# Kernel tuning notes

Hardware: AMD Instinct MI355X
Metric: run time of the kernel (lower is better)

## Reference

```python
import jax, jax.numpy as jnp
import numpy as np

B, T, E, H = 64, 2048, 256, 512


def setup_inputs() -> dict:
    key = jax.random.key(0)
    ks = jax.random.split(key, 8)
    s_in = 1.0 / np.sqrt(E)
    s_h = 1.0 / np.sqrt(H)
    return {
        "x": jax.random.normal(ks[0], (B, T, E), jnp.float32),
        "lengths": jax.random.randint(ks[1], (B,), 1, T + 1, jnp.int32),
        "W_ih": jax.random.normal(ks[2], (H, E), jnp.float32) * s_in,
        "W_hh": jax.random.normal(ks[3], (H, H), jnp.float32) * s_h,
        "b_ih": jax.random.normal(ks[4], (H,), jnp.float32) * s_h,
        "b_hh": jax.random.normal(ks[5], (H,), jnp.float32) * s_h,
        "w_fc": jax.random.normal(ks[6], (1, H), jnp.float32) * s_h,
        "b_fc": jax.random.normal(ks[7], (1,), jnp.float32) * s_h,
    }


def reference(x, lengths, W_ih, W_hh, b_ih, b_hh, w_fc, b_fc):
    # Batched vanilla RNN (tanh), h0 = 0 (init_hidden in the original is dead code).
    b, t, _ = x.shape
    h = W_hh.shape[0]
    # Precompute input projections: [B,T,H] -> scan over time.
    xin = jnp.einsum('bte,he->bth', x, W_ih) + b_ih + b_hh

    def step(h_prev, x_t):
        h_new = jnp.tanh(x_t + h_prev @ W_hh.T)
        return h_new, h_new

    h0 = jnp.zeros((b, h), x.dtype)
    _, hs = jax.lax.scan(step, h0, jnp.swapaxes(xin, 0, 1))  # [T,B,H]
    hs = jnp.swapaxes(hs, 0, 1)  # [B,T,H]

    # fcn: Linear(H,1)+ReLU; count positives over valid (t < length) steps.
    logits = jnp.einsum('bth,oh->bto', hs, w_fc) + b_fc  # [B,T,1]
    valid = (jnp.arange(t)[None, :, None] < lengths[:, None, None])
    outs = jnp.sum((logits > 0) & valid, axis=1).astype(jnp.int32)  # [B,1]

    # h_n: hidden state at the last valid step of each sample.
    idx = jnp.clip(lengths - 1, 0, t - 1)
    h_n = hs[jnp.arange(b), idx]  # [B,H]
    h_n = jnp.where((lengths > 0)[:, None], h_n, jnp.zeros_like(h_n))
    return outs, h_n
```

## Files before the change

kernel.cpp:

```cpp
#include <hip/hip_runtime.h>
#include <stdint.h>

#define BB 64
#define TT 2048
#define EE 256
#define HH 512
#define SLICE 128
#define HXN (BB * 2 * HH)

typedef unsigned long long u64;
typedef float f32x4 __attribute__((ext_vector_type(4)));

__device__ __forceinline__ u64 pack_vt(float v, unsigned tag) {
    return ((u64)tag << 32) | (u64)__float_as_uint(v);
}

__global__ __attribute__((amdgpu_flat_work_group_size(256, 256),
                          amdgpu_waves_per_eu(1, 1)))
void rnn_scan(const float* __restrict__ x,
              const int* __restrict__ lengths,
              const float* __restrict__ W_ih,
              const float* __restrict__ W_hh,
              const float* __restrict__ b_ih,
              const float* __restrict__ b_hh,
              const float* __restrict__ w_fc,
              const float* __restrict__ b_fc,
              float* __restrict__ out,
              u64* __restrict__ hx)
{
    const int b   = blockIdx.x & 63;
    const int s   = blockIdx.x >> 6;
    const int tid = threadIdx.x;
    const int rg  = tid >> 3;
    const int kg  = tid & 7;
    const int row0 = s * SLICE + rg * 4;

    __shared__ float lds_h[2][HH];
    __shared__ float lds_x[2][EE];
    __shared__ float lds_wf[HH];

    f32x4 whh[4][16];
#pragma unroll
    for (int j = 0; j < 4; ++j)
#pragma unroll
        for (int i = 0; i < 16; ++i) {
            const int q = (i + kg) & 15;
            whh[j][i] = *(const f32x4*)&W_hh[(size_t)(row0 + j) * HH + kg * 64 + q * 4];
            asm volatile("" : "+a"(whh[j][i]));
        }
    f32x4 wih[4][8];
#pragma unroll
    for (int j = 0; j < 4; ++j)
#pragma unroll
        for (int i = 0; i < 8; ++i) {
            const int q = (i + kg) & 7;
            wih[j][i] = *(const f32x4*)&W_ih[(size_t)(row0 + j) * EE + kg * 32 + q * 4];
            asm volatile("" : "+v"(wih[j][i]));
        }
    const int pr0 = row0 + (kg & 1) * 2;
    const float bs0 = b_ih[pr0] + b_hh[pr0];
    const float bs1 = b_ih[pr0 + 1] + b_hh[pr0 + 1];
    float bfc = 0.f;
    if (s == 0 && tid < 64) bfc = b_fc[0];
    lds_wf[tid]       = w_fc[tid];
    lds_wf[tid + 256] = w_fc[tid + 256];

    const int len = lengths[b];
    const float* xrow = x + (size_t)b * TT * EE;
    u64* hxb = hx + (size_t)b * 2 * HH;

    lds_h[0][tid]       = 0.f;
    lds_h[0][tid + 256] = 0.f;
    if (tid < 64) *(f32x4*)&lds_x[0][tid * 4] = *(const f32x4*)&xrow[tid * 4];
    __syncthreads();

    int count = 0;

#pragma unroll 1
    for (int t = 0; t < len; ++t) {
        const int p = t & 1;
        const int si = tid - 192;
        f32x4 xn = {0.f, 0.f, 0.f, 0.f};
        if (si >= 0 && t + 1 < TT)
            xn = *(const f32x4*)&xrow[(size_t)(t + 1) * EE + si * 4];

        const float* hb = &lds_h[p][kg * 64];
        const float* xb = &lds_x[p][kg * 32];
        f32x4 a0 = {0.f,0.f,0.f,0.f}, a1 = a0, a2 = a0, a3 = a0;
#define FMA4(acc, w, v) \
        acc[0] = fmaf((w)[0], (v)[0], acc[0]); acc[1] = fmaf((w)[1], (v)[1], acc[1]); \
        acc[2] = fmaf((w)[2], (v)[2], acc[2]); acc[3] = fmaf((w)[3], (v)[3], acc[3]);
#pragma unroll
        for (int i = 0; i < 16; ++i) {
            f32x4 hv = *(const f32x4*)(hb + ((i + kg) & 15) * 4);
            FMA4(a0, whh[0][i], hv) FMA4(a1, whh[1][i], hv)
            FMA4(a2, whh[2][i], hv) FMA4(a3, whh[3][i], hv)
        }
#pragma unroll
        for (int i = 0; i < 8; ++i) {
            f32x4 xv = *(const f32x4*)(xb + ((i + kg) & 7) * 4);
            FMA4(a0, wih[0][i], xv) FMA4(a1, wih[1][i], xv)
            FMA4(a2, wih[2][i], xv) FMA4(a3, wih[3][i], xv)
        }
        float r0 = (a0[0] + a0[1]) + (a0[2] + a0[3]);
        float r1 = (a1[0] + a1[1]) + (a1[2] + a1[3]);
        float r2 = (a2[0] + a2[1]) + (a2[2] + a2[3]);
        float r3 = (a3[0] + a3[1]) + (a3[2] + a3[3]);
#pragma unroll
        for (int m = 1; m < 8; m <<= 1) {
            r0 += __shfl_xor(r0, m); r1 += __shfl_xor(r1, m);
            r2 += __shfl_xor(r2, m); r3 += __shfl_xor(r3, m);
        }

        const unsigned tag = (unsigned)(t + 1);
        u64* slot = hxb + (size_t)p * HH;

        if (kg < 2) {
            const float h0 = tanhf((kg ? r2 : r0) + bs0);
            const float h1 = tanhf((kg ? r3 : r1) + bs1);
            const int gi = pr0;
            *(float2*)&lds_h[p ^ 1][gi] = make_float2(h0, h1);
            __hip_atomic_store(&slot[gi], pack_vt(h0, tag),
                               __ATOMIC_RELAXED, __HIP_MEMORY_SCOPE_AGENT);
            __hip_atomic_store(&slot[gi + 1], pack_vt(h1, tag),
                               __ATOMIC_RELAXED, __HIP_MEMORY_SCOPE_AGENT);
        }

        if (tid < 192) {
            const int sp = (s + 1 + (tid >> 6)) & 3;
            const int gi = sp * SLICE + (tid & 63) * 2;
            u64 v0, v1;
            int g = 0;
            do { v0 = __hip_atomic_load(&slot[gi], __ATOMIC_RELAXED,
                                        __HIP_MEMORY_SCOPE_AGENT);
            } while ((unsigned)(v0 >> 32) != tag && ++g < (1 << 22));
            g = 0;
            do { v1 = __hip_atomic_load(&slot[gi + 1], __ATOMIC_RELAXED,
                                        __HIP_MEMORY_SCOPE_AGENT);
            } while ((unsigned)(v1 >> 32) != tag && ++g < (1 << 22));
            *(float2*)&lds_h[p ^ 1][gi] =
                make_float2(__uint_as_float((unsigned)v0),
                            __uint_as_float((unsigned)v1));
        } else if (t + 1 < TT) {
            *(f32x4*)&lds_x[p ^ 1][si * 4] = xn;
        }
        __syncthreads();

        if (s == 0) {
            if (tid < 64) {
                const f32x4* h4  = (const f32x4*)lds_h[p ^ 1];
                const f32x4* wf4 = (const f32x4*)lds_wf;
                f32x4 v0 = h4[tid * 2], v1 = h4[tid * 2 + 1];
                f32x4 w0 = wf4[tid * 2], w1 = wf4[tid * 2 + 1];
                float pd = v0[0]*w0[0] + v0[1]*w0[1] + v0[2]*w0[2] + v0[3]*w0[3]
                         + v1[0]*w1[0] + v1[1]*w1[1] + v1[2]*w1[2] + v1[3]*w1[3];
#pragma unroll
                for (int m = 1; m < 64; m <<= 1) pd += __shfl_xor(pd, m);
                if (tid == 0 && (pd + bfc) > 0.f) count++;
            }
            if (t == len - 1) {
                *(float2*)&out[64 + b * HH + tid * 2] =
                    *(const float2*)&lds_h[p ^ 1][tid * 2];
            }
        }
    }

    if (s == 0 && tid == 0) out[b] = (float)count;
}

extern "C" void kernel_launch(void* const* d_in, const int* in_sizes, int n_in,
                              void* d_out, int out_size, void* d_ws, size_t ws_size,
                              hipStream_t stream) {
    const float* x       = (const float*)d_in[0];
    const int*   lengths = (const int*)  d_in[1];
    const float* W_ih    = (const float*)d_in[2];
    const float* W_hh    = (const float*)d_in[3];
    const float* b_ih    = (const float*)d_in[4];
    const float* b_hh    = (const float*)d_in[5];
    const float* w_fc    = (const float*)d_in[6];
    const float* b_fc    = (const float*)d_in[7];
    float* out = (float*)d_out;
    u64*   hx  = (u64*)d_ws;

    hipLaunchKernelGGL(rnn_scan, dim3(BB * 4), dim3(256), 0, stream,
                       x, lengths, W_ih, W_hh, b_ih, b_hh, w_fc, b_fc, out, hx);
}
```

Baseline: 6.667 ms.

## Co-locate each batch's slices on one XCD and poll via vectorized L2 loads

At startup each workgroup reads its XCD id and claims a (batch, slice) slot through global atomic counters, so the four slices of a batch tend to land on the same XCD and share its L2. When they do, the per-step hidden-state exchange uses 16-byte stores and sc0 loads that poll both tagged values at once. If polling misses too often, it falls back to the original per-element atomic polling. This adds a bootstrap spin barrier across all 256 workgroups and a memset launch, and assumes every workgroup is resident at the same time.

```diff
diff --git a/kernel.cpp b/kernel.cpp
--- a/kernel.cpp
+++ b/kernel.cpp
@@ -9,10 +9,28 @@
 #define HXN (BB * 2 * HH)
 
 typedef unsigned long long u64;
+typedef u64 u64x2 __attribute__((ext_vector_type(2)));
 typedef float f32x4 __attribute__((ext_vector_type(4)));
 
 __device__ __forceinline__ u64 pack_vt(float v, unsigned tag) {
     return ((u64)tag << 32) | (u64)__float_as_uint(v);
+}
+__device__ __forceinline__ void st_l2_x4(u64* p, u64x2 v) {
+    asm volatile("global_store_dwordx4 %0, %1, off" :: "v"((u64)p), "v"(v) : "memory");
+}
+__device__ __forceinline__ u64x2 ld_l2_x4(const u64* p) {
+    u64x2 v;
+    asm volatile("global_load_dwordx4 %0, %1, off sc0\n\ts_waitcnt vmcnt(0)"
+                 : "=v"(v) : "v"((u64)p) : "memory");
+    return v;
+}
+__device__ __forceinline__ void barrier_lds(void) {
+    asm volatile("s_waitcnt lgkmcnt(0)\n\ts_barrier" ::: "memory");
+}
+
+#define AGENT __HIP_MEMORY_SCOPE_AGENT
+__device__ __forceinline__ unsigned a_add(unsigned* p, unsigned v, int mo) {
+    return __hip_atomic_fetch_add(p, v, mo, AGENT);
 }
 
 __global__ __attribute__((amdgpu_flat_work_group_size(256, 256),
@@ -28,16 +46,56 @@
               float* __restrict__ out,
               u64* __restrict__ hx)
 {
-    const int b   = blockIdx.x & 63;
-    const int s   = blockIdx.x >> 6;
     const int tid = threadIdx.x;
     const int rg  = tid >> 3;
     const int kg  = tid & 7;
-    const int row0 = s * SLICE + rg * 4;
 
     __shared__ float lds_h[2][HH];
     __shared__ float lds_x[2][EE];
     __shared__ float lds_wf[HH];
+    __shared__ int sh_batch, sh_slice, sh_fast, sh_miss;
+
+    if (tid == 0) {
+        unsigned xcd;
+        asm volatile("s_getreg_b32 %0, hwreg(HW_REG_XCC_ID)" : "=s"(xcd));
+        xcd &= 7u;
+        unsigned* boot = (unsigned*)(hx + HXN);
+        unsigned* cnt   = boot;
+        unsigned* total = boot + 8;
+        unsigned* ovfc  = boot + 9;
+        unsigned* bp1   = boot + 16;
+        unsigned* clm   = boot + 80;
+        unsigned my = a_add(&cnt[xcd], 1u, __ATOMIC_RELAXED);
+        int batch = -1, slice = 0, p1 = 0;
+        if (my < 32u) {
+            unsigned slot = xcd * 32u + my;
+            batch = (int)(slot >> 2); slice = (int)(slot & 3u); p1 = 1;
+            __hip_atomic_store(&clm[slot], 1u, __ATOMIC_RELAXED, AGENT);
+            a_add(&bp1[batch], 1u, __ATOMIC_RELAXED);
+        }
+        a_add(total, 1u, __ATOMIC_RELEASE);
+        int g = 0;
+        while (__hip_atomic_load(total, __ATOMIC_ACQUIRE, AGENT) < 256u &&
+               ++g < (1 << 26)) {}
+        if (!p1) {
+            unsigned k = a_add(ovfc, 1u, __ATOMIC_RELAXED);
+            unsigned seen = 0, slot = 0;
+            for (unsigned i2 = 0; i2 < 256u; ++i2) {
+                if (!__hip_atomic_load(&clm[i2], __ATOMIC_RELAXED, AGENT)) {
+                    if (seen == k) { slot = i2; break; }
+                    ++seen;
+                }
+            }
+            batch = (int)(slot >> 2); slice = (int)(slot & 3u);
+        }
+        const int fast =
+            (__hip_atomic_load(&bp1[batch], __ATOMIC_RELAXED, AGENT) == 4u);
+        sh_batch = batch; sh_slice = slice; sh_fast = fast; sh_miss = 0;
+    }
+    __syncthreads();
+    const int b = sh_batch, s = sh_slice;
+    bool fastp = (sh_fast != 0);
+    const int row0 = s * SLICE + rg * 4;
 
     f32x4 whh[4][16];
 #pragma unroll
@@ -120,31 +178,45 @@
             const float h1 = tanhf((kg ? r3 : r1) + bs1);
             const int gi = pr0;
             *(float2*)&lds_h[p ^ 1][gi] = make_float2(h0, h1);
-            __hip_atomic_store(&slot[gi], pack_vt(h0, tag),
-                               __ATOMIC_RELAXED, __HIP_MEMORY_SCOPE_AGENT);
-            __hip_atomic_store(&slot[gi + 1], pack_vt(h1, tag),
-                               __ATOMIC_RELAXED, __HIP_MEMORY_SCOPE_AGENT);
+            const u64 q0 = pack_vt(h0, tag), q1 = pack_vt(h1, tag);
+            u64x2 q; q[0] = q0; q[1] = q1;
+            st_l2_x4(&slot[gi], q);
+            __hip_atomic_store(&slot[gi], q0, __ATOMIC_RELAXED, AGENT);
+            __hip_atomic_store(&slot[gi + 1], q1, __ATOMIC_RELAXED, AGENT);
         }
 
         if (tid < 192) {
             const int sp = (s + 1 + (tid >> 6)) & 3;
             const int gi = sp * SLICE + (tid & 63) * 2;
-            u64 v0, v1;
-            int g = 0;
-            do { v0 = __hip_atomic_load(&slot[gi], __ATOMIC_RELAXED,
-                                        __HIP_MEMORY_SCOPE_AGENT);
-            } while ((unsigned)(v0 >> 32) != tag && ++g < (1 << 22));
-            g = 0;
-            do { v1 = __hip_atomic_load(&slot[gi + 1], __ATOMIC_RELAXED,
-                                        __HIP_MEMORY_SCOPE_AGENT);
-            } while ((unsigned)(v1 >> 32) != tag && ++g < (1 << 22));
+            u64 v0 = 0, v1 = 0;
+            bool ok = false;
+            if (fastp) {
+                for (int g = 0; g < 256; ++g) {
+                    u64x2 v = ld_l2_x4(&slot[gi]);
+                    if ((unsigned)(v[0] >> 32) == tag &&
+                        (unsigned)(v[1] >> 32) == tag) {
+                        v0 = v[0]; v1 = v[1]; ok = true; break;
+                    }
+                }
+                if (!ok) atomicAdd(&sh_miss, 1);
+            }
+            if (!ok) {
+                int g = 0;
+                do { v0 = __hip_atomic_load(&slot[gi], __ATOMIC_RELAXED, AGENT);
+                } while ((unsigned)(v0 >> 32) != tag && ++g < (1 << 22));
+                g = 0;
+                do { v1 = __hip_atomic_load(&slot[gi + 1], __ATOMIC_RELAXED, AGENT);
+                } while ((unsigned)(v1 >> 32) != tag && ++g < (1 << 22));
+            }
             *(float2*)&lds_h[p ^ 1][gi] =
                 make_float2(__uint_as_float((unsigned)v0),
                             __uint_as_float((unsigned)v1));
         } else if (t + 1 < TT) {
             *(f32x4*)&lds_x[p ^ 1][si * 4] = xn;
         }
-        __syncthreads();
+        barrier_lds();
+
+        if (fastp && sh_miss >= 4) fastp = false;
 
         if (s == 0) {
             if (tid < 64) {
@@ -182,6 +254,7 @@
     float* out = (float*)d_out;
     u64*   hx  = (u64*)d_ws;
 
+    hipMemsetAsync((char*)d_ws + (size_t)HXN * 8, 0, 2048, stream);
     hipLaunchKernelGGL(rnn_scan, dim3(BB * 4), dim3(256), 0, stream,
                        x, lengths, W_ih, W_hh, b_ih, b_hh, w_fc, b_fc, out, hx);
 }
```

Result: slower. 7.370 ms (+10.5%).
